# Kernel tuning notes

Hardware: AMD Instinct MI355X
Metric: run time of the kernel (lower is better)

Reference implementation:

```python
import jax, jax.numpy as jnp
import numpy as np

TOP_K = 2
EPS = 0.01
NUM_TOKENS = 262144
NUM_EXPERTS = 128


def setup_inputs() -> dict:
    key = jax.random.key(0)
    router_logits = jax.random.normal(key, (NUM_TOKENS, NUM_EXPERTS), dtype=jnp.float32)
    return {"router_logits": router_logits}


def reference(router_logits):
    logits = router_logits.astype(jnp.float32)
    n_tokens = logits.shape[0]
    rows = jnp.arange(n_tokens)
    neg_inf = jnp.float32(-jnp.inf)

    idx_list, val_list = [], []
    for i in range(TOP_K):
        if i > 0:
            # mask out the previously selected expert (argmax of current logits)
            prev = jnp.argmax(logits, axis=-1)
            logits = logits.at[rows, prev].set(neg_inf)
        max_vals = jnp.max(logits, axis=-1, keepdims=True)   # (T, 1)
        max_idx = jnp.argmax(logits, axis=-1)                # (T,)
        # SparseMixer mask: experts far from the max get -inf before softmax
        mask = (max_vals - logits) / jnp.maximum(jnp.abs(logits), max_vals) > 2.0 * EPS
        masked = jnp.where(mask, neg_inf, logits)
        sm = jax.nn.softmax(masked, axis=-1)                 # (T, E)
        val_list.append(sm[rows, max_idx])
        idx_list.append(max_idx)

    topk_indices = jnp.stack(idx_list, axis=1).astype(jnp.int32)   # (T, top_k)
    topk_values = jnp.stack(val_list, axis=1)                      # (T, top_k)
    return topk_indices, topk_values
```

## Files before the change

### kernel.cpp

```cpp
#include <hip/hip_runtime.h>
#include <math.h>


#define NEXPERTS 128
#define CHUNKS 8

__device__ __forceinline__ void process_token(
    const float4* X, int sub, int token, float* out, int T)
{
    float m1 = -INFINITY, m2 = -INFINITY;
    int   l1 = 0x7fffff, l2 = 0x7fffff;
    #pragma unroll
    for (int c = 0; c < CHUNKS; ++c) {
        const float xs[4] = {X[c].x, X[c].y, X[c].z, X[c].w};
        #pragma unroll
        for (int j = 0; j < 4; ++j) {
            const float xv = xs[j];
            const int   L  = 16 * c + j;
            if (xv > m1)      { m2 = m1; l2 = l1; m1 = xv; l1 = L; }
            else if (xv > m2) { m2 = xv; l2 = L; }
        }
    }
    int i1 = 4 * sub + l1;
    int i2 = 4 * sub + l2;

    #pragma unroll
    for (int off = 2; off > 0; off >>= 1) {
        float om1 = __shfl_xor(m1, off); int oi1 = __shfl_xor(i1, off);
        float om2 = __shfl_xor(m2, off); int oi2 = __shfl_xor(i2, off);
        float w1, ws, lt; int wi1, wis, lti;
        if (om1 > m1 || (om1 == m1 && oi1 < i1)) {
            w1 = om1; wi1 = oi1; ws = om2; wis = oi2; lt = m1;  lti = i1;
        } else {
            w1 = m1;  wi1 = i1;  ws = m2;  wis = i2;  lt = om1; lti = oi1;
        }
        if (lt > ws || (lt == ws && lti < wis)) { m2 = lt; i2 = lti; }
        else                                    { m2 = ws; i2 = wis; }
        m1 = w1; i1 = wi1;
    }
    const float v1 = m1, v2 = m2;
    const int   d  = i1 - 4 * sub;

    float s1 = 0.f, t2 = 0.f;
    #pragma unroll
    for (int c = 0; c < CHUNKS; ++c) {
        const float xs[4] = {X[c].x, X[c].y, X[c].z, X[c].w};
        #pragma unroll
        for (int j = 0; j < 4; ++j) {
            const float xv  = xs[j];
            const int   L   = 16 * c + j;
            const float ax  = fabsf(xv);
            const float num1 = v1 - xv;
            const float num2 = v2 - xv;
            const bool kept1 = !(num1 > 0.02f * fmaxf(ax, v1));
            const bool kept2 = !(num2 > 0.02f * fmaxf(ax, v2));
            const float ev = __expf(-num1);
            if (kept1) s1 += ev;
            float t = kept2 ? ev : 0.f;
            if (L == d) t = 0.f;
            t2 += t;
        }
    }
    #pragma unroll
    for (int off = 2; off > 0; off >>= 1) {
        s1 += __shfl_xor(s1, off);
        t2 += __shfl_xor(t2, off);
    }

    if (sub == 0) {
        const float s2 = t2 * __expf(v1 - v2);
        out[(size_t)token * 2 + 0] = (float)i1;
        out[(size_t)token * 2 + 1] = (float)i2;
        float* vals = out + (size_t)2 * T;
        vals[(size_t)token * 2 + 0] = 1.0f / s1;
        vals[(size_t)token * 2 + 1] = 1.0f / s2;
    }
}

__global__ __launch_bounds__(256, 4) void sparsemixer_route_kernel(
    const float* __restrict__ logits,
    float* __restrict__ out,
    int T)
{
    const int tid = blockIdx.x * blockDim.x + threadIdx.x;
    const int grp = tid >> 2;
    const int sub = threadIdx.x & 3;
    const int G   = (gridDim.x * blockDim.x) >> 2;
    const int t0  = grp;
    const int t1  = grp + G;

    float4 X0[CHUNKS], X1[CHUNKS];
    if (t0 < T) {
        const float4* p0 = reinterpret_cast<const float4*>(logits + (size_t)t0 * NEXPERTS);
        #pragma unroll
        for (int c = 0; c < CHUNKS; ++c) X0[c] = p0[sub + c * 4];
    }
    if (t1 < T) {
        const float4* p1 = reinterpret_cast<const float4*>(logits + (size_t)t1 * NEXPERTS);
        #pragma unroll
        for (int c = 0; c < CHUNKS; ++c) X1[c] = p1[sub + c * 4];
    }

    if (t0 < T) process_token(X0, sub, t0, out, T);
    if (t1 < T) process_token(X1, sub, t1, out, T);
}

extern "C" void kernel_launch(void* const* d_in, const int* in_sizes, int n_in,
                              void* d_out, int out_size, void* d_ws, size_t ws_size,
                              hipStream_t stream) {
    const float* logits = (const float*)d_in[0];
    float* out = (float*)d_out;
    const int T = in_sizes[0] / NEXPERTS;

    const int blocks = (T + 127) / 128;
    sparsemixer_route_kernel<<<blocks, 256, 0, stream>>>(logits, out, T);
}
```

Baseline: 32.39 us.

## Process four tokens per thread group with double-buffered loads and simplified mask

```diff
diff --git a/kernel.cpp b/kernel.cpp
--- a/kernel.cpp
+++ b/kernel.cpp
@@ -4,9 +4,17 @@
 
 #define NEXPERTS 128
 #define CHUNKS 8
+#define INV098 1.0204082f
 
-__device__ __forceinline__ void process_token(
-    const float4* X, int sub, int token, float* out, int T)
+__device__ __forceinline__ void load_row(float4* X, const float* logits,
+                                         int token, int sub) {
+    const float4* p = reinterpret_cast<const float4*>(logits + (size_t)token * NEXPERTS);
+    #pragma unroll
+    for (int c = 0; c < CHUNKS; ++c) X[c] = p[sub + c * 4];
+}
+
+__device__ __forceinline__ void process_token(const float4* X, int sub,
+                                              int token, float* out, int T)
 {
     float m1 = -INFINITY, m2 = -INFINITY;
     int   l1 = 0x7fffff, l2 = 0x7fffff;
@@ -39,7 +47,9 @@
         m1 = w1; i1 = wi1;
     }
     const float v1 = m1, v2 = m2;
-    const int   d  = i1 - 4 * sub;
+
+    const float th1 = v1 * (v1 >= 0.f ? 0.98f : INV098);
+    const float th2 = v2 * (v2 >= 0.f ? 0.98f : INV098);
 
     float s1 = 0.f, t2 = 0.f;
     #pragma unroll
@@ -47,18 +57,10 @@
         const float xs[4] = {X[c].x, X[c].y, X[c].z, X[c].w};
         #pragma unroll
         for (int j = 0; j < 4; ++j) {
-            const float xv  = xs[j];
-            const int   L   = 16 * c + j;
-            const float ax  = fabsf(xv);
-            const float num1 = v1 - xv;
-            const float num2 = v2 - xv;
-            const bool kept1 = !(num1 > 0.02f * fmaxf(ax, v1));
-            const bool kept2 = !(num2 > 0.02f * fmaxf(ax, v2));
-            const float ev = __expf(-num1);
-            if (kept1) s1 += ev;
-            float t = kept2 ? ev : 0.f;
-            if (L == d) t = 0.f;
-            t2 += t;
+            const float xv = xs[j];
+            const float ev = __expf(xv - v1);
+            if (xv >= th1) s1 += ev;
+            if (xv >= th2) t2 += ev;
         }
     }
     #pragma unroll
@@ -68,7 +70,7 @@
     }
 
     if (sub == 0) {
-        const float s2 = t2 * __expf(v1 - v2);
+        const float s2 = (t2 - 1.0f) * __expf(v1 - v2);
         out[(size_t)token * 2 + 0] = (float)i1;
         out[(size_t)token * 2 + 1] = (float)i2;
         float* vals = out + (size_t)2 * T;
@@ -86,23 +88,19 @@
     const int grp = tid >> 2;
     const int sub = threadIdx.x & 3;
     const int G   = (gridDim.x * blockDim.x) >> 2;
-    const int t0  = grp;
-    const int t1  = grp + G;
 
-    float4 X0[CHUNKS], X1[CHUNKS];
-    if (t0 < T) {
-        const float4* p0 = reinterpret_cast<const float4*>(logits + (size_t)t0 * NEXPERTS);
-        #pragma unroll
-        for (int c = 0; c < CHUNKS; ++c) X0[c] = p0[sub + c * 4];
-    }
-    if (t1 < T) {
-        const float4* p1 = reinterpret_cast<const float4*>(logits + (size_t)t1 * NEXPERTS);
-        #pragma unroll
-        for (int c = 0; c < CHUNKS; ++c) X1[c] = p1[sub + c * 4];
-    }
+    float4 A[CHUNKS], B[CHUNKS];
 
-    if (t0 < T) process_token(X0, sub, t0, out, T);
-    if (t1 < T) process_token(X1, sub, t1, out, T);
+    const int t0 = grp, t1 = grp + G, t2_ = grp + 2 * G, t3 = grp + 3 * G;
+
+    if (t0 < T) load_row(A, logits, t0, sub);
+    if (t1 < T) load_row(B, logits, t1, sub);
+    if (t0 < T) process_token(A, sub, t0, out, T);
+    if (t2_ < T) load_row(A, logits, t2_, sub);
+    if (t1 < T) process_token(B, sub, t1, out, T);
+    if (t3 < T) load_row(B, logits, t3, sub);
+    if (t2_ < T) process_token(A, sub, t2_, out, T);
+    if (t3 < T) process_token(B, sub, t3, out, T);
 }
 
 extern "C" void kernel_launch(void* const* d_in, const int* in_sizes, int n_in,
@@ -112,6 +110,6 @@
     float* out = (float*)d_out;
     const int T = in_sizes[0] / NEXPERTS;
 
-    const int blocks = (T + 127) / 128;
+    const int blocks = (T + 255) / 256;
     sparsemixer_route_kernel<<<blocks, 256, 0, stream>>>(logits, out, T);
 }
```

Measured after the change: 32.82 us. About the same (+1.3%).
